# Performance work log

Measured on AMD Instinct MI355X. Metric: run time of the kernel, lower is better.

## Reference

```python
import jax, jax.numpy as jnp
import numpy as np

N_NODES = 100000
N_EDGES = 1200000
D_IN = 64
D_HID = 64


def setup_inputs() -> dict:
    key = jax.random.key(0)
    k1, k2, k3, k4 = jax.random.split(key, 4)
    x = jax.random.normal(k1, (N_NODES, D_IN), dtype=jnp.float32)
    edge_index = jax.random.randint(k2, (2, N_EDGES), 0, N_NODES, dtype=jnp.int32)
    edge_attr = jax.random.uniform(k3, (N_EDGES,), dtype=jnp.float32)
    W = jax.random.normal(k4, (D_HID, D_IN), dtype=jnp.float32) / np.sqrt(D_IN)
    b = jnp.zeros((D_HID,), dtype=jnp.float32)
    return {"x": x, "edge_index": edge_index, "edge_attr": edge_attr, "W": W, "b": b}


def _gcn_conv(x, edge_index, edge_weight, W, b):
    # PyG GCNConv: add self-loops (weight 1), symmetric normalization,
    # linear transform, scatter-add aggregation at target (col), bias.
    n = x.shape[0]
    loop = jnp.arange(n, dtype=edge_index.dtype)
    row = jnp.concatenate([edge_index[0], loop])  # source
    col = jnp.concatenate([edge_index[1], loop])  # target
    ew = jnp.concatenate([edge_weight, jnp.ones((n,), edge_weight.dtype)])
    deg = jax.ops.segment_sum(ew, col, num_segments=n)  # [N]
    dis = jnp.where(deg > 0, jax.lax.rsqrt(deg), 0.0)
    norm = dis[row] * ew * dis[col]                     # [E+N]
    h = x @ W.T                                          # [N, D_HID]
    msg = norm[:, None] * h[row]                         # [E+N, D_HID]
    out = jax.ops.segment_sum(msg, col, num_segments=n)  # [N, D_HID]
    return out + b


def reference(x, edge_index, edge_attr, W, b):
    # layer_num=2 -> single GCNConv; dropout is identity in eval mode.
    h = _gcn_conv(x, edge_index, edge_attr, W, b)
    return jax.nn.relu(h)
```

## Files before the change

kernel.cpp:

```cpp
#include <hip/hip_runtime.h>

#define N_NODES 100000
#define N_EDGES 1200000
#define D 64
#define KP 68
#define TN 64
#define CAP 48
#define Q15 32767.0f
#define INVQ15 (1.0f / 32767.0f)
#define BW 512
#define BSH 9
#define NBKT ((N_NODES + BW - 1) / BW)
#define CAPB 8192
#define N4 (N_EDGES / 4)
#define NB_COARSE ((N4 + 511) / 512)
#define NB_GEMM ((N_NODES + TN - 1) / TN)

__device__ __forceinline__ unsigned short f2bf(float f) {
    unsigned u = __float_as_uint(f);
    return (unsigned short)((u + 0x7FFFu + ((u >> 16) & 1u)) >> 16);
}
__device__ __forceinline__ float bf2f(unsigned short h) {
    return __uint_as_float((unsigned)h << 16);
}

__global__ __launch_bounds__(256) void k_pre(const int4* __restrict__ row4,
                                             const int4* __restrict__ col4,
                                             const float4* __restrict__ ew4,
                                             int* __restrict__ gcur,
                                             int2* __restrict__ coarse,
                                             const float* __restrict__ x,
                                             const float* __restrict__ W,
                                             unsigned short* __restrict__ hb,
                                             int n4, int n_nodes) {
    __shared__ int lcnt[NBKT];
    __shared__ int lbase[NBKT];
    __shared__ float wt[D * KP];
    int t = threadIdx.x;

    if (blockIdx.x < NB_COARSE) {
        for (int i = t; i < NBKT; i += 256) lcnt[i] = 0;
        __syncthreads();

        int bkt[8]; int slot[8]; int2 rec[8];
        #pragma unroll
        for (int k = 0; k < 8; k++) bkt[k] = -1;

        #pragma unroll
        for (int r = 0; r < 2; r++) {
            int q = blockIdx.x * 512 + r * 256 + t;
            if (q < n4) {
                int4 rr = row4[q]; int4 cc = col4[q]; float4 ww = ew4[q];
                int j = r * 4;
                int c;
                c = cc.x; bkt[j+0] = c >> BSH;
                rec[j+0] = make_int2(rr.x, ((c & (BW-1)) << 15) | (int)(ww.x * Q15 + 0.5f));
                slot[j+0] = atomicAdd(&lcnt[bkt[j+0]], 1);
                c = cc.y; bkt[j+1] = c >> BSH;
                rec[j+1] = make_int2(rr.y, ((c & (BW-1)) << 15) | (int)(ww.y * Q15 + 0.5f));
                slot[j+1] = atomicAdd(&lcnt[bkt[j+1]], 1);
                c = cc.z; bkt[j+2] = c >> BSH;
                rec[j+2] = make_int2(rr.z, ((c & (BW-1)) << 15) | (int)(ww.z * Q15 + 0.5f));
                slot[j+2] = atomicAdd(&lcnt[bkt[j+2]], 1);
                c = cc.w; bkt[j+3] = c >> BSH;
                rec[j+3] = make_int2(rr.w, ((c & (BW-1)) << 15) | (int)(ww.w * Q15 + 0.5f));
                slot[j+3] = atomicAdd(&lcnt[bkt[j+3]], 1);
            }
        }
        __syncthreads();
        for (int i = t; i < NBKT; i += 256) {
            int c = lcnt[i];
            lbase[i] = c ? atomicAdd(&gcur[i], c) : 0;
        }
        __syncthreads();
        #pragma unroll
        for (int k = 0; k < 8; k++) {
            if (bkt[k] >= 0) {
                int pos = lbase[bkt[k]] + slot[k];
                if (pos < CAPB) coarse[(size_t)bkt[k] * CAPB + pos] = rec[k];
            }
        }
    } else {
        int base = (blockIdx.x - NB_COARSE) * TN;
        #pragma unroll
        for (int c = 0; c < 16; c++) {
            int idx = t + c * 256;
            wt[(idx & 63) * KP + (idx >> 6)] = W[idx];
        }
        __syncthreads();

        int tx = t & 15, ty = t >> 4;
        int f0 = tx * 4, n0 = base + ty * 4;
        const float* xr0 = x + (size_t)min(n0 + 0, n_nodes - 1) * D;
        const float* xr1 = x + (size_t)min(n0 + 1, n_nodes - 1) * D;
        const float* xr2 = x + (size_t)min(n0 + 2, n_nodes - 1) * D;
        const float* xr3 = x + (size_t)min(n0 + 3, n_nodes - 1) * D;

        float acc[4][4] = {};
        #pragma unroll 4
        for (int k = 0; k < D; k += 4) {
            float a[4][4], wv[4][4];
            *(float4*)a[0] = *(const float4*)&xr0[k];
            *(float4*)a[1] = *(const float4*)&xr1[k];
            *(float4*)a[2] = *(const float4*)&xr2[k];
            *(float4*)a[3] = *(const float4*)&xr3[k];
            #pragma unroll
            for (int kk = 0; kk < 4; kk++)
                *(float4*)wv[kk] = *(const float4*)&wt[(k + kk) * KP + f0];
            #pragma unroll
            for (int kk = 0; kk < 4; kk++)
                #pragma unroll
                for (int j = 0; j < 4; j++)
                    #pragma unroll
                    for (int ff = 0; ff < 4; ff++)
                        acc[j][ff] = fmaf(a[j][kk], wv[kk][ff], acc[j][ff]);
        }
        #pragma unroll
        for (int j = 0; j < 4; j++) {
            int n = n0 + j;
            if (n < n_nodes) {
                unsigned short h0 = f2bf(acc[j][0]);
                unsigned short h1 = f2bf(acc[j][1]);
                unsigned short h2 = f2bf(acc[j][2]);
                unsigned short h3 = f2bf(acc[j][3]);
                uint2 pk;
                pk.x = (unsigned)h0 | ((unsigned)h1 << 16);
                pk.y = (unsigned)h2 | ((unsigned)h3 << 16);
                *(uint2*)&hb[(size_t)n * D + f0] = pk;
            }
        }
    }
}

__global__ __launch_bounds__(512) void k_bin(const int* __restrict__ gcur,
                                             const int2* __restrict__ coarse,
                                             int* __restrict__ cnt,
                                             float* __restrict__ dis,
                                             unsigned int* __restrict__ em, int n_nodes) {
    __shared__ int   cur512[BW];
    __shared__ float d512[BW];
    int b = blockIdx.x, t = threadIdx.x;
    int total = min(gcur[b], CAPB);
    int nbase = b * BW;
    int bw = min(BW, n_nodes - nbase);
    for (int i = t; i < BW; i += 512) { cur512[i] = 0; d512[i] = 0.f; }
    __syncthreads();
    const int2* src = &coarse[(size_t)b * CAPB];
    for (int i = t; i < total; i += 512) {
        int2 r = src[i];
        int cl = (r.y >> 15) & (BW - 1);
        float w = (float)(r.y & 0x7FFF) * INVQ15;
        int s = atomicAdd(&cur512[cl], 1);
        atomicAdd(&d512[cl], w);
        if (s < CAP)
            em[(size_t)(nbase + cl) * CAP + s] = ((unsigned)r.x << 15) | (unsigned)(r.y & 0x7FFF);
    }
    __syncthreads();
    for (int i = t; i < bw; i += 512) {
        cnt[nbase + i] = cur512[i];
        dis[nbase + i] = rsqrtf(1.0f + d512[i]);
    }
}

__global__ __launch_bounds__(256) void k_agg_cap(const int* __restrict__ cnt,
                                                 const unsigned int* __restrict__ em,
                                                 const unsigned short* __restrict__ hb,
                                                 const float* __restrict__ dis,
                                                 const float* __restrict__ b,
                                                 float* __restrict__ out, int n_nodes) {
    int w = threadIdx.x >> 6, l = threadIdx.x & 63;
    int n0 = blockIdx.x * 8 + w * 2;
    int n1 = n0 + 1;
    int c0 = min(cnt[n0], CAP);
    int c1 = min(cnt[n1], CAP);
    int recs0 = (int)em[(size_t)n0 * CAP + min(l, max(c0 - 1, 0))];
    int recs1 = (int)em[(size_t)n1 * CAP + min(l, max(c1 - 1, 0))];
    float ds0 = dis[n0], ds1 = dis[n1];
    float acc0 = ds0 * bf2f(hb[(size_t)n0 * D + l]);
    float acc1 = ds1 * bf2f(hb[(size_t)n1 * D + l]);

    int i0 = 0, i1 = 0;
    while (i0 + 4 <= c0 && i1 + 4 <= c1) {
        unsigned a0 = (unsigned)__shfl(recs0, i0 + 0);
        unsigned a1 = (unsigned)__shfl(recs0, i0 + 1);
        unsigned a2 = (unsigned)__shfl(recs0, i0 + 2);
        unsigned a3 = (unsigned)__shfl(recs0, i0 + 3);
        unsigned b0 = (unsigned)__shfl(recs1, i1 + 0);
        unsigned b1 = (unsigned)__shfl(recs1, i1 + 1);
        unsigned b2 = (unsigned)__shfl(recs1, i1 + 2);
        unsigned b3 = (unsigned)__shfl(recs1, i1 + 3);
        float ha0 = bf2f(hb[(size_t)(a0 >> 15) * D + l]);
        float ha1 = bf2f(hb[(size_t)(a1 >> 15) * D + l]);
        float ha2 = bf2f(hb[(size_t)(a2 >> 15) * D + l]);
        float ha3 = bf2f(hb[(size_t)(a3 >> 15) * D + l]);
        float hb0 = bf2f(hb[(size_t)(b0 >> 15) * D + l]);
        float hb1 = bf2f(hb[(size_t)(b1 >> 15) * D + l]);
        float hb2 = bf2f(hb[(size_t)(b2 >> 15) * D + l]);
        float hb3 = bf2f(hb[(size_t)(b3 >> 15) * D + l]);
        float wa0 = (float)(a0 & 0x7FFFu) * INVQ15 * dis[a0 >> 15];
        float wa1 = (float)(a1 & 0x7FFFu) * INVQ15 * dis[a1 >> 15];
        float wa2 = (float)(a2 & 0x7FFFu) * INVQ15 * dis[a2 >> 15];
        float wa3 = (float)(a3 & 0x7FFFu) * INVQ15 * dis[a3 >> 15];
        float wb0 = (float)(b0 & 0x7FFFu) * INVQ15 * dis[b0 >> 15];
        float wb1 = (float)(b1 & 0x7FFFu) * INVQ15 * dis[b1 >> 15];
        float wb2 = (float)(b2 & 0x7FFFu) * INVQ15 * dis[b2 >> 15];
        float wb3 = (float)(b3 & 0x7FFFu) * INVQ15 * dis[b3 >> 15];
        acc0 = fmaf(wa0, ha0, acc0);
        acc0 = fmaf(wa1, ha1, acc0);
        acc0 = fmaf(wa2, ha2, acc0);
        acc0 = fmaf(wa3, ha3, acc0);
        acc1 = fmaf(wb0, hb0, acc1);
        acc1 = fmaf(wb1, hb1, acc1);
        acc1 = fmaf(wb2, hb2, acc1);
        acc1 = fmaf(wb3, hb3, acc1);
        i0 += 4; i1 += 4;
    }
    for (; i0 + 4 <= c0; i0 += 4) {
        unsigned a0 = (unsigned)__shfl(recs0, i0 + 0);
        unsigned a1 = (unsigned)__shfl(recs0, i0 + 1);
        unsigned a2 = (unsigned)__shfl(recs0, i0 + 2);
        unsigned a3 = (unsigned)__shfl(recs0, i0 + 3);
        float ha0 = bf2f(hb[(size_t)(a0 >> 15) * D + l]);
        float ha1 = bf2f(hb[(size_t)(a1 >> 15) * D + l]);
        float ha2 = bf2f(hb[(size_t)(a2 >> 15) * D + l]);
        float ha3 = bf2f(hb[(size_t)(a3 >> 15) * D + l]);
        acc0 = fmaf((float)(a0 & 0x7FFFu) * INVQ15 * dis[a0 >> 15], ha0, acc0);
        acc0 = fmaf((float)(a1 & 0x7FFFu) * INVQ15 * dis[a1 >> 15], ha1, acc0);
        acc0 = fmaf((float)(a2 & 0x7FFFu) * INVQ15 * dis[a2 >> 15], ha2, acc0);
        acc0 = fmaf((float)(a3 & 0x7FFFu) * INVQ15 * dis[a3 >> 15], ha3, acc0);
    }
    for (; i0 < c0; i0++) {
        unsigned a = (unsigned)__shfl(recs0, i0);
        acc0 = fmaf((float)(a & 0x7FFFu) * INVQ15 * dis[a >> 15],
                    bf2f(hb[(size_t)(a >> 15) * D + l]), acc0);
    }
    for (; i1 + 4 <= c1; i1 += 4) {
        unsigned b0 = (unsigned)__shfl(recs1, i1 + 0);
        unsigned b1 = (unsigned)__shfl(recs1, i1 + 1);
        unsigned b2 = (unsigned)__shfl(recs1, i1 + 2);
        unsigned b3 = (unsigned)__shfl(recs1, i1 + 3);
        float hb0 = bf2f(hb[(size_t)(b0 >> 15) * D + l]);
        float hb1 = bf2f(hb[(size_t)(b1 >> 15) * D + l]);
        float hb2 = bf2f(hb[(size_t)(b2 >> 15) * D + l]);
        float hb3 = bf2f(hb[(size_t)(b3 >> 15) * D + l]);
        acc1 = fmaf((float)(b0 & 0x7FFFu) * INVQ15 * dis[b0 >> 15], hb0, acc1);
        acc1 = fmaf((float)(b1 & 0x7FFFu) * INVQ15 * dis[b1 >> 15], hb1, acc1);
        acc1 = fmaf((float)(b2 & 0x7FFFu) * INVQ15 * dis[b2 >> 15], hb2, acc1);
        acc1 = fmaf((float)(b3 & 0x7FFFu) * INVQ15 * dis[b3 >> 15], hb3, acc1);
    }
    for (; i1 < c1; i1++) {
        unsigned bb = (unsigned)__shfl(recs1, i1);
        acc1 = fmaf((float)(bb & 0x7FFFu) * INVQ15 * dis[bb >> 15],
                    bf2f(hb[(size_t)(bb >> 15) * D + l]), acc1);
    }

    float bl = b[l];
    float v0 = fmaf(ds0, acc0, bl);
    float v1 = fmaf(ds1, acc1, bl);
    out[(size_t)n0 * D + l] = v0 > 0.f ? v0 : 0.f;
    out[(size_t)n1 * D + l] = v1 > 0.f ? v1 : 0.f;
}

extern "C" void kernel_launch(void* const* d_in, const int* in_sizes, int n_in,
                              void* d_out, int out_size, void* d_ws, size_t ws_size,
                              hipStream_t stream) {
    const float* x   = (const float*)d_in[0];
    const int*   ei  = (const int*)d_in[1];
    const float* ew  = (const float*)d_in[2];
    const float* W   = (const float*)d_in[3];
    const float* b   = (const float*)d_in[4];
    float* out = (float*)d_out;

    const int* row = ei;
    const int* col = ei + N_EDGES;

    char* p = (char*)d_ws;
    auto carve = [&](size_t bytes) { char* q = p; p += (bytes + 255) & ~(size_t)255; return q; };
    float*          dis    = (float*)carve(N_NODES * sizeof(float));
    unsigned short* hb     = (unsigned short*)carve((size_t)N_NODES * D * sizeof(unsigned short));
    int*            cnt    = (int*)  carve(N_NODES * sizeof(int));
    unsigned int*   em     = (unsigned int*)carve((size_t)N_NODES * CAP * sizeof(unsigned int));
    int*            gcur   = (int*)  carve(NBKT * sizeof(int));
    int2*           coarse = (int2*) carve((size_t)NBKT * CAPB * sizeof(int2));

    hipMemsetAsync(gcur, 0, NBKT * sizeof(int), stream);

    k_pre<<<NB_COARSE + NB_GEMM, 256, 0, stream>>>(
        (const int4*)row, (const int4*)col, (const float4*)ew, gcur, coarse,
        x, W, hb, N4, N_NODES);
    k_bin<<<NBKT, 512, 0, stream>>>(gcur, coarse, cnt, dis, em, N_NODES);
    k_agg_cap<<<N_NODES / 8, 256, 0, stream>>>(cnt, em, hb, dis, b, out, N_NODES);
}
```

Measured before the change: 167.5 us.

## Locally sort edge records by bucket in LDS before coalesced scatter

```diff
diff --git a/kernel.cpp b/kernel.cpp
--- a/kernel.cpp
+++ b/kernel.cpp
@@ -39,6 +39,8 @@
     int t = threadIdx.x;
 
     if (blockIdx.x < NB_COARSE) {
+        int2* sorted = (int2*)wt;
+        int*  bofs   = (int*)((char*)wt + 16384);
         for (int i = t; i < NBKT; i += 256) lcnt[i] = 0;
         __syncthreads();
 
@@ -52,33 +54,49 @@
             if (q < n4) {
                 int4 rr = row4[q]; int4 cc = col4[q]; float4 ww = ew4[q];
                 int j = r * 4;
-                int c;
-                c = cc.x; bkt[j+0] = c >> BSH;
-                rec[j+0] = make_int2(rr.x, ((c & (BW-1)) << 15) | (int)(ww.x * Q15 + 0.5f));
-                slot[j+0] = atomicAdd(&lcnt[bkt[j+0]], 1);
-                c = cc.y; bkt[j+1] = c >> BSH;
-                rec[j+1] = make_int2(rr.y, ((c & (BW-1)) << 15) | (int)(ww.y * Q15 + 0.5f));
-                slot[j+1] = atomicAdd(&lcnt[bkt[j+1]], 1);
-                c = cc.z; bkt[j+2] = c >> BSH;
-                rec[j+2] = make_int2(rr.z, ((c & (BW-1)) << 15) | (int)(ww.z * Q15 + 0.5f));
-                slot[j+2] = atomicAdd(&lcnt[bkt[j+2]], 1);
-                c = cc.w; bkt[j+3] = c >> BSH;
-                rec[j+3] = make_int2(rr.w, ((c & (BW-1)) << 15) | (int)(ww.w * Q15 + 0.5f));
-                slot[j+3] = atomicAdd(&lcnt[bkt[j+3]], 1);
+                int c, bk;
+                c = cc.x; bk = c >> BSH; bkt[j+0] = bk;
+                rec[j+0] = make_int2(rr.x, (bk << 24) | ((c & (BW-1)) << 15) | (int)(ww.x * Q15 + 0.5f));
+                slot[j+0] = atomicAdd(&lcnt[bk], 1);
+                c = cc.y; bk = c >> BSH; bkt[j+1] = bk;
+                rec[j+1] = make_int2(rr.y, (bk << 24) | ((c & (BW-1)) << 15) | (int)(ww.y * Q15 + 0.5f));
+                slot[j+1] = atomicAdd(&lcnt[bk], 1);
+                c = cc.z; bk = c >> BSH; bkt[j+2] = bk;
+                rec[j+2] = make_int2(rr.z, (bk << 24) | ((c & (BW-1)) << 15) | (int)(ww.z * Q15 + 0.5f));
+                slot[j+2] = atomicAdd(&lcnt[bk], 1);
+                c = cc.w; bk = c >> BSH; bkt[j+3] = bk;
+                rec[j+3] = make_int2(rr.w, (bk << 24) | ((c & (BW-1)) << 15) | (int)(ww.w * Q15 + 0.5f));
+                slot[j+3] = atomicAdd(&lcnt[bk], 1);
             }
         }
         __syncthreads();
         for (int i = t; i < NBKT; i += 256) {
             int c = lcnt[i];
             lbase[i] = c ? atomicAdd(&gcur[i], c) : 0;
-        }
-        __syncthreads();
-        #pragma unroll
-        for (int k = 0; k < 8; k++) {
-            if (bkt[k] >= 0) {
-                int pos = lbase[bkt[k]] + slot[k];
-                if (pos < CAPB) coarse[(size_t)bkt[k] * CAPB + pos] = rec[k];
-            }
+            bofs[i] = c;
+        }
+        __syncthreads();
+        for (int d = 1; d < NBKT; d <<= 1) {
+            int v = 0;
+            if (t < NBKT && t >= d) v = bofs[t - d];
+            __syncthreads();
+            if (t < NBKT && t >= d) bofs[t] += v;
+            __syncthreads();
+        }
+        if (t < NBKT) bofs[t] -= lcnt[t];
+        __syncthreads();
+
+        #pragma unroll
+        for (int k = 0; k < 8; k++)
+            if (bkt[k] >= 0) sorted[bofs[bkt[k]] + slot[k]] = rec[k];
+        __syncthreads();
+
+        int m = bofs[NBKT - 1] + lcnt[NBKT - 1];
+        for (int i = t; i < m; i += 256) {
+            int2 r = sorted[i];
+            int bk = ((unsigned)r.y) >> 24;
+            int pos = lbase[bk] + (i - bofs[bk]);
+            if (pos < CAPB) coarse[(size_t)bk * CAPB + pos] = r;
         }
     } else {
         int base = (blockIdx.x - NB_COARSE) * TN;
@@ -132,21 +150,21 @@
     }
 }
 
-__global__ __launch_bounds__(512) void k_bin(const int* __restrict__ gcur,
-                                             const int2* __restrict__ coarse,
-                                             int* __restrict__ cnt,
-                                             float* __restrict__ dis,
-                                             unsigned int* __restrict__ em, int n_nodes) {
+__global__ __launch_bounds__(1024) void k_bin(const int* __restrict__ gcur,
+                                              const int2* __restrict__ coarse,
+                                              int* __restrict__ cnt,
+                                              float* __restrict__ dis,
+                                              unsigned int* __restrict__ em, int n_nodes) {
     __shared__ int   cur512[BW];
     __shared__ float d512[BW];
     int b = blockIdx.x, t = threadIdx.x;
     int total = min(gcur[b], CAPB);
     int nbase = b * BW;
     int bw = min(BW, n_nodes - nbase);
-    for (int i = t; i < BW; i += 512) { cur512[i] = 0; d512[i] = 0.f; }
+    for (int i = t; i < BW; i += 1024) { cur512[i] = 0; d512[i] = 0.f; }
     __syncthreads();
     const int2* src = &coarse[(size_t)b * CAPB];
-    for (int i = t; i < total; i += 512) {
+    for (int i = t; i < total; i += 1024) {
         int2 r = src[i];
         int cl = (r.y >> 15) & (BW - 1);
         float w = (float)(r.y & 0x7FFF) * INVQ15;
@@ -156,15 +174,20 @@
             em[(size_t)(nbase + cl) * CAP + s] = ((unsigned)r.x << 15) | (unsigned)(r.y & 0x7FFF);
     }
     __syncthreads();
-    for (int i = t; i < bw; i += 512) {
+    for (int i = t; i < bw; i += 1024) {
         cnt[nbase + i] = cur512[i];
         dis[nbase + i] = rsqrtf(1.0f + d512[i]);
     }
 }
 
+#define AGG_STEP(rec, accv)                                                          \
+    {                                                                                \
+        float hh = bf2f(hsb[(size_t)((rec) >> 15) * D + l]);                         \
+        accv = fmaf((float)((rec) & 0x7FFFu) * INVQ15 * dis[(rec) >> 15], hh, accv); \
+    }
 __global__ __launch_bounds__(256) void k_agg_cap(const int* __restrict__ cnt,
                                                  const unsigned int* __restrict__ em,
-                                                 const unsigned short* __restrict__ hb,
+                                                 const unsigned short* __restrict__ hsb,
                                                  const float* __restrict__ dis,
                                                  const float* __restrict__ b,
                                                  float* __restrict__ out, int n_nodes) {
@@ -176,8 +199,8 @@
     int recs0 = (int)em[(size_t)n0 * CAP + min(l, max(c0 - 1, 0))];
     int recs1 = (int)em[(size_t)n1 * CAP + min(l, max(c1 - 1, 0))];
     float ds0 = dis[n0], ds1 = dis[n1];
-    float acc0 = ds0 * bf2f(hb[(size_t)n0 * D + l]);
-    float acc1 = ds1 * bf2f(hb[(size_t)n1 * D + l]);
+    float acc0 = ds0 * bf2f(hsb[(size_t)n0 * D + l]);
+    float acc1 = ds1 * bf2f(hsb[(size_t)n1 * D + l]);
 
     int i0 = 0, i1 = 0;
     while (i0 + 4 <= c0 && i1 + 4 <= c1) {
@@ -189,14 +212,14 @@
         unsigned b1 = (unsigned)__shfl(recs1, i1 + 1);
         unsigned b2 = (unsigned)__shfl(recs1, i1 + 2);
         unsigned b3 = (unsigned)__shfl(recs1, i1 + 3);
-        float ha0 = bf2f(hb[(size_t)(a0 >> 15) * D + l]);
-        float ha1 = bf2f(hb[(size_t)(a1 >> 15) * D + l]);
-        float ha2 = bf2f(hb[(size_t)(a2 >> 15) * D + l]);
-        float ha3 = bf2f(hb[(size_t)(a3 >> 15) * D + l]);
-        float hb0 = bf2f(hb[(size_t)(b0 >> 15) * D + l]);
-        float hb1 = bf2f(hb[(size_t)(b1 >> 15) * D + l]);
-        float hb2 = bf2f(hb[(size_t)(b2 >> 15) * D + l]);
-        float hb3 = bf2f(hb[(size_t)(b3 >> 15) * D + l]);
+        float ha0 = bf2f(hsb[(size_t)(a0 >> 15) * D + l]);
+        float ha1 = bf2f(hsb[(size_t)(a1 >> 15) * D + l]);
+        float ha2 = bf2f(hsb[(size_t)(a2 >> 15) * D + l]);
+        float ha3 = bf2f(hsb[(size_t)(a3 >> 15) * D + l]);
+        float hb0 = bf2f(hsb[(size_t)(b0 >> 15) * D + l]);
+        float hb1 = bf2f(hsb[(size_t)(b1 >> 15) * D + l]);
+        float hb2 = bf2f(hsb[(size_t)(b2 >> 15) * D + l]);
+        float hb3 = bf2f(hsb[(size_t)(b3 >> 15) * D + l]);
         float wa0 = (float)(a0 & 0x7FFFu) * INVQ15 * dis[a0 >> 15];
         float wa1 = (float)(a1 & 0x7FFFu) * INVQ15 * dis[a1 >> 15];
         float wa2 = (float)(a2 & 0x7FFFu) * INVQ15 * dis[a2 >> 15];
@@ -220,10 +243,10 @@
         unsigned a1 = (unsigned)__shfl(recs0, i0 + 1);
         unsigned a2 = (unsigned)__shfl(recs0, i0 + 2);
         unsigned a3 = (unsigned)__shfl(recs0, i0 + 3);
-        float ha0 = bf2f(hb[(size_t)(a0 >> 15) * D + l]);
-        float ha1 = bf2f(hb[(size_t)(a1 >> 15) * D + l]);
-        float ha2 = bf2f(hb[(size_t)(a2 >> 15) * D + l]);
-        float ha3 = bf2f(hb[(size_t)(a3 >> 15) * D + l]);
+        float ha0 = bf2f(hsb[(size_t)(a0 >> 15) * D + l]);
+        float ha1 = bf2f(hsb[(size_t)(a1 >> 15) * D + l]);
+        float ha2 = bf2f(hsb[(size_t)(a2 >> 15) * D + l]);
+        float ha3 = bf2f(hsb[(size_t)(a3 >> 15) * D + l]);
         acc0 = fmaf((float)(a0 & 0x7FFFu) * INVQ15 * dis[a0 >> 15], ha0, acc0);
         acc0 = fmaf((float)(a1 & 0x7FFFu) * INVQ15 * dis[a1 >> 15], ha1, acc0);
         acc0 = fmaf((float)(a2 & 0x7FFFu) * INVQ15 * dis[a2 >> 15], ha2, acc0);
@@ -231,18 +254,17 @@
     }
     for (; i0 < c0; i0++) {
         unsigned a = (unsigned)__shfl(recs0, i0);
-        acc0 = fmaf((float)(a & 0x7FFFu) * INVQ15 * dis[a >> 15],
-                    bf2f(hb[(size_t)(a >> 15) * D + l]), acc0);
+        AGG_STEP(a, acc0);
     }
     for (; i1 + 4 <= c1; i1 += 4) {
         unsigned b0 = (unsigned)__shfl(recs1, i1 + 0);
         unsigned b1 = (unsigned)__shfl(recs1, i1 + 1);
         unsigned b2 = (unsigned)__shfl(recs1, i1 + 2);
         unsigned b3 = (unsigned)__shfl(recs1, i1 + 3);
-        float hb0 = bf2f(hb[(size_t)(b0 >> 15) * D + l]);
-        float hb1 = bf2f(hb[(size_t)(b1 >> 15) * D + l]);
-        float hb2 = bf2f(hb[(size_t)(b2 >> 15) * D + l]);
-        float hb3 = bf2f(hb[(size_t)(b3 >> 15) * D + l]);
+        float hb0 = bf2f(hsb[(size_t)(b0 >> 15) * D + l]);
+        float hb1 = bf2f(hsb[(size_t)(b1 >> 15) * D + l]);
+        float hb2 = bf2f(hsb[(size_t)(b2 >> 15) * D + l]);
+        float hb3 = bf2f(hsb[(size_t)(b3 >> 15) * D + l]);
         acc1 = fmaf((float)(b0 & 0x7FFFu) * INVQ15 * dis[b0 >> 15], hb0, acc1);
         acc1 = fmaf((float)(b1 & 0x7FFFu) * INVQ15 * dis[b1 >> 15], hb1, acc1);
         acc1 = fmaf((float)(b2 & 0x7FFFu) * INVQ15 * dis[b2 >> 15], hb2, acc1);
@@ -250,8 +272,7 @@
     }
     for (; i1 < c1; i1++) {
         unsigned bb = (unsigned)__shfl(recs1, i1);
-        acc1 = fmaf((float)(bb & 0x7FFFu) * INVQ15 * dis[bb >> 15],
-                    bf2f(hb[(size_t)(bb >> 15) * D + l]), acc1);
+        AGG_STEP(bb, acc1);
     }
 
     float bl = b[l];
@@ -288,6 +309,6 @@
     k_pre<<<NB_COARSE + NB_GEMM, 256, 0, stream>>>(
         (const int4*)row, (const int4*)col, (const float4*)ew, gcur, coarse,
         x, W, hb, N4, N_NODES);
-    k_bin<<<NBKT, 512, 0, stream>>>(gcur, coarse, cnt, dis, em, N_NODES);
+    k_bin<<<NBKT, 1024, 0, stream>>>(gcur, coarse, cnt, dis, em, N_NODES);
     k_agg_cap<<<N_NODES / 8, 256, 0, stream>>>(cnt, em, hb, dis, b, out, N_NODES);
 }
```

Result: no change. 164.8 us (median of 2 runs) (-1.6%).
